# Kernel tuning notes

Hardware: AMD Instinct MI355X
Metric: run time of the kernel (lower is better)

Reference implementation:

```python
import jax, jax.numpy as jnp
import numpy as np

N, E_RAW, F_IN, H, C = 50000, 800000, 500, 5, 32
HID = H * C  # 160
NEG_GAT = 0.2   # GATConv leaky_relu slope for attention logits
NEG = 0.01      # F.leaky_relu default slope
LN_EPS = 1e-5


def glorot(key, shape):
    fan_in, fan_out = shape[0], shape[-1]
    lim = jnp.sqrt(6.0 / (fan_in + fan_out))
    return jax.random.uniform(key, shape, jnp.float32, -lim, lim)


def setup_inputs() -> dict:
    key = jax.random.key(0)
    ks = jax.random.split(key, 12)
    x = jax.random.normal(ks[0], (N, F_IN), jnp.float32)
    edge_index = jax.random.randint(ks[1], (2, E_RAW), 0, N, jnp.int64)
    return {
        "x": x,
        "edge_index": edge_index,
        "W1": glorot(ks[2], (F_IN, HID)),
        "att1_s": glorot(ks[3], (H, C)),
        "att1_d": glorot(ks[4], (H, C)),
        "b1": jnp.zeros((HID,), jnp.float32),
        "g1": jnp.ones((HID,), jnp.float32),
        "be1": jnp.zeros((HID,), jnp.float32),
        "W2": glorot(ks[5], (HID, HID)),
        "att2_s": glorot(ks[6], (H, C)),
        "att2_d": glorot(ks[7], (H, C)),
        "b2": jnp.zeros((HID,), jnp.float32),
        "Wm": glorot(ks[8], (HID, HID)),
        "bm": jnp.zeros((HID,), jnp.float32),
    }


def add_self_loops(edge_index):
    loops = jnp.arange(N, dtype=edge_index.dtype)
    return jnp.concatenate([edge_index, jnp.stack([loops, loops])], axis=1)


def gat_conv(x, src, dst, W, att_s, att_d, bias):
    # x: [N, Fin] -> per-head transform [N, H, C]
    xl = (x @ W).reshape(N, H, C)
    a_s = jnp.einsum('nhc,hc->nh', xl, att_s)  # [N, H]
    a_d = jnp.einsum('nhc,hc->nh', xl, att_d)
    logits = jax.nn.leaky_relu(a_s[src] + a_d[dst], NEG_GAT)  # [E, H]
    # segment softmax over incoming edges of each dst node
    lmax = jax.ops.segment_max(logits, dst, num_segments=N)
    alpha = jnp.exp(logits - lmax[dst])
    denom = jax.ops.segment_sum(alpha, dst, num_segments=N)
    alpha = alpha / (denom[dst] + 1e-16)
    msg = xl[src] * alpha[:, :, None]  # [E, H, C]
    out = jax.ops.segment_sum(msg, dst, num_segments=N)
    return out.reshape(N, HID) + bias, alpha


def layer_norm(x, g, b):
    mu = jnp.mean(x, axis=-1, keepdims=True)
    var = jnp.mean((x - mu) ** 2, axis=-1, keepdims=True)
    return (x - mu) * jax.lax.rsqrt(var + LN_EPS) * g + b


def reference(x, edge_index, W1, att1_s, att1_d, b1, g1, be1,
              W2, att2_s, att2_d, b2, Wm, bm):
    ei = add_self_loops(edge_index)
    src, dst = ei[0], ei[1]
    h, alpha1 = gat_conv(x, src, dst, W1, att1_s, att1_d, b1)
    h = jax.nn.leaky_relu(h, NEG)
    h = layer_norm(h, g1, be1)  # dropout is identity in eval mode
    h, alpha2 = gat_conv(h, src, dst, W2, att2_s, att2_d, b2)
    h = jax.nn.leaky_relu(h, NEG)
    out = jax.nn.leaky_relu(h @ Wm + bm, NEG)
    return out, alpha1, alpha2
```

## Files before the change

### kernel.cpp

```cpp
#include <hip/hip_runtime.h>

#define N_NODES 50000
#define E_RAW_N 800000
#define E_TOT   850000
#define F_IN_K  500
#define HID     160
#define XSTR    184

using short8 = __attribute__((ext_vector_type(8))) short;
using f32x4  = __attribute__((ext_vector_type(4))) float;

__device__ __forceinline__ float b2f(unsigned short u) {
  union { unsigned int i; float f; } v; v.i = ((unsigned int)u) << 16; return v.f;
}
__device__ __forceinline__ unsigned short f2b(float f) {
  union { float f; unsigned int i; } v; v.f = f;
  unsigned int i = v.i;
  unsigned int lsb = (i >> 16) & 1u;
  i += 0x7fffu + lsb;
  return (unsigned short)(i >> 16);
}

__device__ __forceinline__ float wsum(float x) {
  #pragma unroll
  for (int o = 32; o; o >>= 1) x += __shfl_xor(x, o, 64);
  return x;
}
__device__ __forceinline__ float wmax(float x) {
  #pragma unroll
  for (int o = 32; o; o >>= 1) x = fmaxf(x, __shfl_xor(x, o, 64));
  return x;
}
__device__ __forceinline__ float lrelu2(float x) { return x > 0.f ? x : 0.2f * x; }

__global__ void detect_kernel(const int* __restrict__ ei, int* __restrict__ flag) {
  if (threadIdx.x == 0 && blockIdx.x == 0) {
    int allz = 1;
    for (int i = 1; i < 128; i += 2) if (ei[i] != 0) { allz = 0; break; }
    *flag = allz;
  }
}
__device__ __forceinline__ int edge_src(const int* ei, int wide, int e) {
  return wide ? ei[2 * e] : ei[e];
}
__device__ __forceinline__ int edge_dst(const int* ei, int wide, int e) {
  return wide ? ei[2 * (E_RAW_N + e)] : ei[E_RAW_N + e];
}

__global__ __launch_bounds__(256) void convert_all(
    const float* __restrict__ W1, const float* __restrict__ W2, const float* __restrict__ Wm,
    unsigned short* __restrict__ Bt1, unsigned short* __restrict__ Bt2,
    unsigned short* __restrict__ Btm)
{
  const int i = blockIdx.x * 256 + threadIdx.x;
  if (i < HID * 512) {
    const int c = i / 512, k = i % 512;
    Bt1[i] = f2b((k < F_IN_K) ? W1[(long)k * HID + c] : 0.f);
  }
  if (i < HID * 192) {
    const int c = i / 192, k = i % 192;
    Bt2[i] = f2b((k < HID) ? W2[(long)k * HID + c] : 0.f);
    Btm[i] = f2b((k < HID) ? Wm[(long)k * HID + c] : 0.f);
  }
}

template<typename AT, int K, int KPAD, int BK, int MODE>
__global__ __launch_bounds__(128) void gemm_lds(
    const AT* __restrict__ A, const unsigned short* __restrict__ Bt,
    float* __restrict__ C, unsigned short* __restrict__ Ch,
    const float* __restrict__ bias,
    const float* __restrict__ att_s, const float* __restrict__ att_d,
    float* __restrict__ a_d)
{
  constexpr bool AB16 = (sizeof(AT) == 2);
  constexpr int LSTR = BK + 8;
  constexpr int CHUNKS = KPAD / BK;
  constexpr int KSC = BK / 32;
  constexpr int ROWU = BK / 8;
  constexpr int UNITS = HID * ROWU;
  static_assert(UNITS % 128 == 0, "units must tile threads");
  constexpr int UPT = UNITS / 128;
  __shared__ __align__(16) unsigned short Bs[HID][LSTR];

  const int t = threadIdx.x;
  const int l = t & 63;
  const int w = t >> 6;
  const int m = l & 15;
  const int kgrp = (l >> 4) * 8;
  const int rbase = blockIdx.x * 32 + w * 16;
  const int arow = (rbase + m < N_NODES) ? rbase + m : N_NODES - 1;
  const AT* Arow = A + (long)arow * K;

  f32x4 acc[10];
  #pragma unroll
  for (int i = 0; i < 10; ++i) acc[i] = (f32x4){0.f, 0.f, 0.f, 0.f};

  short8 rb[UPT];
  float  arF[KSC][8], arF2[KSC][8];
  short8 arS[KSC], arS2[KSC];

  auto loadB = [&](int cc, short8* dst) {
    #pragma unroll
    for (int i = 0; i < UPT; ++i) {
      const int u = i * 128 + t;
      const int c = u / ROWU;
      const int k8 = u % ROWU;
      dst[i] = *(const short8*)(Bt + (long)c * KPAD + cc * BK + k8 * 8);
    }
  };
  auto loadA = [&](int cc, float aF[KSC][8], short8* aS) {
    #pragma unroll
    for (int ks = 0; ks < KSC; ++ks) {
      const int kb = cc * BK + ks * 32 + kgrp;
      if constexpr (AB16) {
        short8 v = (short8){0,0,0,0,0,0,0,0};
        if (kb + 8 <= K) v = *(const short8*)(Arow + kb);
        else if (kb < K) {
          #pragma unroll
          for (int j = 0; j < 8; ++j) v[j] = (kb + j < K) ? (short)Arow[kb + j] : (short)0;
        }
        aS[ks] = v;
      } else {
        if (kb + 8 <= K) {
          const float4 a0 = *(const float4*)(Arow + kb);
          const float4 a1 = *(const float4*)(Arow + kb + 4);
          aF[ks][0]=a0.x; aF[ks][1]=a0.y; aF[ks][2]=a0.z; aF[ks][3]=a0.w;
          aF[ks][4]=a1.x; aF[ks][5]=a1.y; aF[ks][6]=a1.z; aF[ks][7]=a1.w;
        } else {
          #pragma unroll
          for (int j = 0; j < 8; ++j) aF[ks][j] = (kb + j < K) ? (float)Arow[kb + j] : 0.f;
        }
      }
    }
  };

  loadB(0, rb);
  loadA(0, arF, arS);

  for (int cc = 0; cc < CHUNKS; ++cc) {
    __syncthreads();
    #pragma unroll
    for (int i = 0; i < UPT; ++i) {
      const int u = i * 128 + t;
      const int c = u / ROWU;
      const int k8 = u % ROWU;
      *(short8*)&Bs[c][k8 * 8] = rb[i];
    }
    __syncthreads();
    if (cc + 1 < CHUNKS) {
      loadB(cc + 1, rb);
      loadA(cc + 1, arF2, arS2);
      __builtin_amdgcn_sched_barrier(0);
    }
    __builtin_amdgcn_s_setprio(1);
    #pragma unroll
    for (int ks = 0; ks < KSC; ++ks) {
      short8 ah;
      if constexpr (AB16) {
        ah = arS[ks];
      } else {
        #pragma unroll
        for (int j = 0; j < 8; ++j) ah[j] = (short)f2b(arF[ks][j]);
      }
      #pragma unroll
      for (int ct = 0; ct < 10; ++ct) {
        const short8 bh = *(const short8*)&Bs[ct * 16 + m][ks * 32 + kgrp];
        acc[ct] = __builtin_amdgcn_mfma_f32_16x16x32_bf16(ah, bh, acc[ct], 0, 0, 0);
      }
    }
    __builtin_amdgcn_s_setprio(0);
    if (cc + 1 < CHUNKS) {
      #pragma unroll
      for (int ks = 0; ks < KSC; ++ks) {
        if constexpr (AB16) arS[ks] = arS2[ks];
        else {
          #pragma unroll
          for (int j = 0; j < 8; ++j) arF[ks][j] = arF2[ks][j];
        }
      }
    }
  }

  const int crow0 = rbase + (l >> 4) * 4;

  if (MODE == 2) {
    #pragma unroll
    for (int r = 0; r < 4; ++r) {
      float ps[5], pd[5];
      #pragma unroll
      for (int h = 0; h < 5; ++h) {
        float s = acc[2*h][r]     * att_s[(2*h) * 16 + m]
                + acc[2*h + 1][r] * att_s[(2*h + 1) * 16 + m];
        float d = acc[2*h][r]     * att_d[(2*h) * 16 + m]
                + acc[2*h + 1][r] * att_d[(2*h + 1) * 16 + m];
        #pragma unroll
        for (int o = 1; o < 16; o <<= 1) {
          s += __shfl_xor(s, o, 64);
          d += __shfl_xor(d, o, 64);
        }
        ps[h] = s; pd[h] = d;
      }
      const int crow = crow0 + r;
      if (crow < N_NODES && m < 5) {
        const float vs = m == 0 ? ps[0] : m == 1 ? ps[1] : m == 2 ? ps[2] : m == 3 ? ps[3] : ps[4];
        const float vd = m == 0 ? pd[0] : m == 1 ? pd[1] : m == 2 ? pd[2] : m == 3 ? pd[3] : pd[4];
        ((float*)(Ch + (long)crow * XSTR + 160))[m] = vs;
        a_d[crow * 5 + m] = vd;
      }
    }
  }

  #pragma unroll
  for (int r = 0; r < 4; ++r) {
    const int crow = crow0 + r;
    if (crow < N_NODES) {
      #pragma unroll
      for (int ct = 0; ct < 10; ++ct) {
        const int col = ct * 16 + m;
        float v = acc[ct][r];
        if (MODE == 1) { v += bias[col]; v = v > 0.f ? v : 0.01f * v; }
        if (MODE == 2) Ch[(long)crow * XSTR + col] = f2b(v);
        else           C[(long)crow * HID + col] = v;
      }
    }
  }
}

__global__ __launch_bounds__(256) void count_kernel(const int* __restrict__ ei,
    const int* __restrict__ flag, int* __restrict__ deg) {
  const int e = blockIdx.x * 256 + threadIdx.x;
  if (e >= E_TOT) return;
  const int wide = *flag;
  const int d = (e < E_RAW_N) ? edge_dst(ei, wide, e) : (e - E_RAW_N);
  atomicAdd(&deg[d], 1);
}

#define SCAN_CHUNK 49
__global__ __launch_bounds__(1024) void scan_kernel(const int* __restrict__ deg, int* __restrict__ off) {
  __shared__ int wtot[16];
  const int t = threadIdx.x;
  const int lane = t & 63, wid = t >> 6;
  const int base = t * SCAN_CHUNK;
  int local[SCAN_CHUNK];
  int sum = 0;
  #pragma unroll
  for (int i = 0; i < SCAN_CHUNK; ++i) {
    const int idx = base + i;
    const int v = (idx < N_NODES) ? deg[idx] : 0;
    local[i] = sum;
    sum += v;
  }
  int inc = sum;
  #pragma unroll
  for (int o = 1; o < 64; o <<= 1) {
    const int y = __shfl_up(inc, o, 64);
    if (lane >= o) inc += y;
  }
  if (lane == 63) wtot[wid] = inc;
  __syncthreads();
  if (wid == 0 && lane < 16) {
    const int v = wtot[lane];
    int inc2 = v;
    #pragma unroll
    for (int o = 1; o < 16; o <<= 1) {
      const int y = __shfl_up(inc2, o, 64);
      if (lane >= o) inc2 += y;
    }
    wtot[lane] = inc2 - v;
  }
  __syncthreads();
  const int pre = wtot[wid] + (inc - sum);
  #pragma unroll
  for (int i = 0; i < SCAN_CHUNK; ++i) {
    const int idx = base + i;
    if (idx < N_NODES) off[idx] = pre + local[i];
  }
  if (t == 1023) off[N_NODES] = E_TOT;
}

__global__ __launch_bounds__(256) void fill_kernel(const int* __restrict__ ei,
    const int* __restrict__ flag, const int* __restrict__ off,
    int* __restrict__ fillc, int* __restrict__ csr_src, int* __restrict__ csr_eid) {
  const int e = blockIdx.x * 256 + threadIdx.x;
  if (e >= E_TOT) return;
  const int wide = *flag;
  int s, d;
  if (e < E_RAW_N) { s = edge_src(ei, wide, e); d = edge_dst(ei, wide, e); }
  else { s = e - E_RAW_N; d = s; }
  const int p = off[d] + atomicAdd(&fillc[d], 1);
  csr_src[p] = s;
  csr_eid[p] = e;
}

template<int DO_LN>
__global__ __launch_bounds__(256) void node_kernel(
    const int* __restrict__ off_, const int* __restrict__ csr_src, const int* __restrict__ csr_eid,
    const unsigned short* __restrict__ xlh,
    const float* __restrict__ a_d,
    float* __restrict__ alpha_out,
    const float* __restrict__ bias,
    const float* __restrict__ gamma_, const float* __restrict__ beta_,
    unsigned short* __restrict__ hout)
{
  __shared__ int   srcS[4][64];
  __shared__ float alS[4][64][6];

  const int w = threadIdx.x >> 6;
  const int l = threadIdx.x & 63;
  const int n = blockIdx.x * 4 + w;
  if (n >= N_NODES) return;
  const int off = off_[n];
  const int deg = off_[n + 1] - off;

  const float ad0 = a_d[n*5+0], ad1 = a_d[n*5+1], ad2 = a_d[n*5+2], ad3 = a_d[n*5+3], ad4 = a_d[n*5+4];
  const int hA = l >> 4;
  float accx = 0.f, accy = 0.f, accz = 0.f;

  if (deg <= 64) {
    int src = 0, eid = 0;
    float e0 = 0.f, e1 = 0.f, e2 = 0.f, e3 = 0.f, e4 = 0.f;
    if (l < deg) {
      src = csr_src[off + l];
      eid = csr_eid[off + l];
      const float* ap = (const float*)(xlh + (unsigned)src * XSTR + 160);
      e0 = __expf(lrelu2(ap[0] + ad0));
      e1 = __expf(lrelu2(ap[1] + ad1));
      e2 = __expf(lrelu2(ap[2] + ad2));
      e3 = __expf(lrelu2(ap[3] + ad3));
      e4 = __expf(lrelu2(ap[4] + ad4));
    }
    const float i0 = 1.f / (wsum(e0) + 1e-16f), i1 = 1.f / (wsum(e1) + 1e-16f),
                i2 = 1.f / (wsum(e2) + 1e-16f), i3 = 1.f / (wsum(e3) + 1e-16f),
                i4 = 1.f / (wsum(e4) + 1e-16f);
    const float a0 = e0 * i0, a1 = e1 * i1, a2 = e2 * i2, a3 = e3 * i3, a4 = e4 * i4;
    if (l < deg) {
      float* aw = alpha_out + (long)eid * 5;
      aw[0] = a0; aw[1] = a1; aw[2] = a2; aw[3] = a3; aw[4] = a4;
    }
    srcS[w][l] = src;
    alS[w][l][0] = a0; alS[w][l][1] = a1; alS[w][l][2] = a2;
    alS[w][l][3] = a3; alS[w][l][4] = a4;

    const int degR = (deg + 7) & ~7;
    const unsigned cx = 2 * l, cz = 128 + l;
    for (int s0 = 0; s0 < degR; s0 += 8) {
      int sr[8]; float aA[8], aB[8];
      #pragma unroll
      for (int j = 0; j < 8; ++j) {
        sr[j] = srcS[w][s0 + j];
        aA[j] = alS[w][s0 + j][hA];
        aB[j] = alS[w][s0 + j][4];
      }
      ushort2 u2[8]; unsigned short z[8];
      #pragma unroll
      for (int j = 0; j < 8; ++j) {
        const unsigned xb = (unsigned)sr[j] * XSTR;
        u2[j] = *(const ushort2*)(xlh + xb + cx);
        if (l < 32) z[j] = xlh[xb + cz];
      }
      #pragma unroll
      for (int j = 0; j < 8; ++j) {
        accx += b2f(u2[j].x) * aA[j];
        accy += b2f(u2[j].y) * aA[j];
        if (l < 32) accz += b2f(z[j]) * aB[j];
      }
    }
  } else {
    float m0 = -1e30f, m1 = -1e30f, m2 = -1e30f, m3 = -1e30f, m4 = -1e30f;
    for (int s = l; s < deg; s += 64) {
      const float* ap = (const float*)(xlh + (unsigned)csr_src[off + s] * XSTR + 160);
      m0 = fmaxf(m0, lrelu2(ap[0] + ad0));
      m1 = fmaxf(m1, lrelu2(ap[1] + ad1));
      m2 = fmaxf(m2, lrelu2(ap[2] + ad2));
      m3 = fmaxf(m3, lrelu2(ap[3] + ad3));
      m4 = fmaxf(m4, lrelu2(ap[4] + ad4));
    }
    m0 = wmax(m0); m1 = wmax(m1); m2 = wmax(m2); m3 = wmax(m3); m4 = wmax(m4);
    float s0 = 0.f, s1 = 0.f, s2 = 0.f, s3 = 0.f, s4 = 0.f;
    for (int s = l; s < deg; s += 64) {
      const float* ap = (const float*)(xlh + (unsigned)csr_src[off + s] * XSTR + 160);
      s0 += __expf(lrelu2(ap[0] + ad0) - m0);
      s1 += __expf(lrelu2(ap[1] + ad1) - m1);
      s2 += __expf(lrelu2(ap[2] + ad2) - m2);
      s3 += __expf(lrelu2(ap[3] + ad3) - m3);
      s4 += __expf(lrelu2(ap[4] + ad4) - m4);
    }
    const float i0 = 1.f / (wsum(s0) + 1e-16f), i1 = 1.f / (wsum(s1) + 1e-16f),
                i2 = 1.f / (wsum(s2) + 1e-16f), i3 = 1.f / (wsum(s3) + 1e-16f),
                i4 = 1.f / (wsum(s4) + 1e-16f);
    const float adA = hA == 0 ? ad0 : hA == 1 ? ad1 : hA == 2 ? ad2 : ad3;
    const float mA  = hA == 0 ? m0  : hA == 1 ? m1  : hA == 2 ? m2  : m3;
    const float iA  = hA == 0 ? i0  : hA == 1 ? i1  : hA == 2 ? i2  : i3;
    float adw = 0.f, mw = 0.f, iw = 0.f;
    if (l < 5) {
      adw = l == 0 ? ad0 : l == 1 ? ad1 : l == 2 ? ad2 : l == 3 ? ad3 : ad4;
      mw  = l == 0 ? m0  : l == 1 ? m1  : l == 2 ? m2  : l == 3 ? m3  : m4;
      iw  = l == 0 ? i0  : l == 1 ? i1  : l == 2 ? i2  : l == 3 ? i3  : i4;
    }
    for (int s = 0; s < deg; ++s) {
      const int p = off + s;
      const int srcs = csr_src[p];
      const unsigned xb = (unsigned)srcs * XSTR;
      const float* ap = (const float*)(xlh + xb + 160);
      const float aA = __expf(lrelu2(ap[hA] + adA) - mA) * iA;
      const ushort2 u2 = *(const ushort2*)(xlh + xb + 2 * l);
      accx += b2f(u2.x) * aA;
      accy += b2f(u2.y) * aA;
      if (l < 32) {
        const float aC = __expf(lrelu2(ap[4] + ad4) - m4) * i4;
        accz += b2f(xlh[xb + 128 + l]) * aC;
      }
      if (l < 5) {
        alpha_out[(long)csr_eid[p] * 5 + l] = __expf(lrelu2(ap[l] + adw) - mw) * iw;
      }
    }
  }

  const int c0 = 2 * l, c2 = 128 + l;
  float v0 = accx + bias[c0];     v0 = v0 > 0.f ? v0 : 0.01f * v0;
  float v1 = accy + bias[c0 + 1]; v1 = v1 > 0.f ? v1 : 0.01f * v1;
  float v2 = 0.f;
  if (l < 32) { v2 = accz + bias[c2]; v2 = v2 > 0.f ? v2 : 0.01f * v2; }

  const long hb = (long)n * HID;
  if (DO_LN) {
    const float tot = wsum(v0 + v1 + v2);
    const float mean = tot * (1.f / 160.f);
    const float d0 = v0 - mean, d1 = v1 - mean;
    float sq = d0 * d0 + d1 * d1;
    float d2 = 0.f;
    if (l < 32) { d2 = v2 - mean; sq += d2 * d2; }
    const float var = wsum(sq) * (1.f / 160.f);
    const float rstd = rsqrtf(var + 1e-5f);
    hout[hb + c0]     = f2b(d0 * rstd * gamma_[c0]     + beta_[c0]);
    hout[hb + c0 + 1] = f2b(d1 * rstd * gamma_[c0 + 1] + beta_[c0 + 1]);
    if (l < 32) hout[hb + c2] = f2b(d2 * rstd * gamma_[c2] + beta_[c2]);
  } else {
    hout[hb + c0]     = f2b(v0);
    hout[hb + c0 + 1] = f2b(v1);
    if (l < 32) hout[hb + c2] = f2b(v2);
  }
}

extern "C" void kernel_launch(void* const* d_in, const int* in_sizes, int n_in,
                              void* d_out, int out_size, void* d_ws, size_t ws_size,
                              hipStream_t stream)
{
  const float* x     = (const float*)d_in[0];
  const int*   ei    = (const int*)d_in[1];
  const float* W1    = (const float*)d_in[2];
  const float* att1s = (const float*)d_in[3];
  const float* att1d = (const float*)d_in[4];
  const float* b1    = (const float*)d_in[5];
  const float* g1    = (const float*)d_in[6];
  const float* be1   = (const float*)d_in[7];
  const float* W2    = (const float*)d_in[8];
  const float* att2s = (const float*)d_in[9];
  const float* att2d = (const float*)d_in[10];
  const float* b2    = (const float*)d_in[11];
  const float* Wm    = (const float*)d_in[12];
  const float* bm    = (const float*)d_in[13];

  float* out    = (float*)d_out;
  float* alpha1 = out + (long)N_NODES * HID;
  float* alpha2 = alpha1 + (long)E_TOT * 5;

  char* p = (char*)d_ws;
  auto alloc = [&](size_t bytes) { void* r = (void*)p; p += (bytes + 255) & ~(size_t)255; return r; };
  unsigned short* hb16 = (unsigned short*)alloc((size_t)N_NODES * HID * 2);
  unsigned short* xlh  = (unsigned short*)alloc((size_t)N_NODES * XSTR * 2);
  float* ad_  = (float*)alloc((size_t)N_NODES * 5 * 4);
  int* deg    = (int*)alloc((size_t)N_NODES * 4);
  int* fillc  = (int*)alloc((size_t)N_NODES * 4);
  int* off    = (int*)alloc((size_t)(N_NODES + 1) * 4);
  int* csrS   = (int*)alloc((size_t)E_TOT * 4);
  int* csrE   = (int*)alloc((size_t)E_TOT * 4);
  int* flag   = (int*)alloc(256);
  unsigned short* Bt1 = (unsigned short*)alloc((size_t)HID * 512 * 2);
  unsigned short* Bt2 = (unsigned short*)alloc((size_t)HID * 192 * 2);
  unsigned short* Btm = (unsigned short*)alloc((size_t)HID * 192 * 2);

  hipMemsetAsync(deg, 0, (size_t)N_NODES * 4, stream);
  hipMemsetAsync(fillc, 0, (size_t)N_NODES * 4, stream);

  detect_kernel<<<1, 64, 0, stream>>>(ei, flag);
  const int EB = (E_TOT + 255) / 256;
  count_kernel<<<EB, 256, 0, stream>>>(ei, flag, deg);
  scan_kernel<<<1, 1024, 0, stream>>>(deg, off);
  fill_kernel<<<EB, 256, 0, stream>>>(ei, flag, off, fillc, csrS, csrE);

  convert_all<<<(HID * 512 + 255) / 256, 256, 0, stream>>>(W1, W2, Wm, Bt1, Bt2, Btm);

  const int GB = (N_NODES + 31) / 32;

  gemm_lds<float, F_IN_K, 512, 64, 2><<<GB, 128, 0, stream>>>(x, Bt1, nullptr, xlh, nullptr, att1s, att1d, ad_);
  node_kernel<1><<<N_NODES / 4, 256, 0, stream>>>(off, csrS, csrE, xlh, ad_, alpha1, b1, g1, be1, hb16);

  gemm_lds<unsigned short, HID, 192, 64, 2><<<GB, 128, 0, stream>>>(hb16, Bt2, nullptr, xlh, nullptr, att2s, att2d, ad_);
  node_kernel<0><<<N_NODES / 4, 256, 0, stream>>>(off, csrS, csrE, xlh, ad_, alpha2, b2, nullptr, nullptr, hb16);

  gemm_lds<unsigned short, HID, 192, 64, 1><<<GB, 128, 0, stream>>>(hb16, Btm, out, nullptr, bm, nullptr, nullptr, nullptr);
}
```

Measured before the change: 398.8 us.

## Split GEMM output columns across two wave groups with 256-thread blocks

The LDS-tiled GEMM now launches 256 threads per block. Four waves are arranged as two row groups by two column groups, and each wave computes 5 of the 10 column tiles instead of all 10. This halves the per-wave accumulator count and MFMA chain and doubles the waves per block, aiming for more latency hiding and less register pressure. In return, each A row is loaded twice, and the attention-logit dot products are now partial sums. Those partials are combined through shared memory behind an extra barrier.

```diff
diff --git a/kernel.cpp b/kernel.cpp
--- a/kernel.cpp
+++ b/kernel.cpp
@@ -65,7 +65,7 @@
 }
 
 template<typename AT, int K, int KPAD, int BK, int MODE>
-__global__ __launch_bounds__(128) void gemm_lds(
+__global__ __launch_bounds__(256) void gemm_lds(
     const AT* __restrict__ A, const unsigned short* __restrict__ Bt,
     float* __restrict__ C, unsigned short* __restrict__ Ch,
     const float* __restrict__ bias,
@@ -78,22 +78,25 @@
   constexpr int KSC = BK / 32;
   constexpr int ROWU = BK / 8;
   constexpr int UNITS = HID * ROWU;
-  static_assert(UNITS % 128 == 0, "units must tile threads");
-  constexpr int UPT = UNITS / 128;
+  static_assert(UNITS % 256 == 0, "units must tile threads");
+  constexpr int UPT = UNITS / 256;
   __shared__ __align__(16) unsigned short Bs[HID][LSTR];
+  __shared__ float attP[32][6][2];
 
   const int t = threadIdx.x;
   const int l = t & 63;
   const int w = t >> 6;
+  const int rg = w & 1;
+  const int cg = w >> 1;
   const int m = l & 15;
   const int kgrp = (l >> 4) * 8;
-  const int rbase = blockIdx.x * 32 + w * 16;
+  const int rbase = blockIdx.x * 32 + rg * 16;
   const int arow = (rbase + m < N_NODES) ? rbase + m : N_NODES - 1;
   const AT* Arow = A + (long)arow * K;
 
-  f32x4 acc[10];
-  #pragma unroll
-  for (int i = 0; i < 10; ++i) acc[i] = (f32x4){0.f, 0.f, 0.f, 0.f};
+  f32x4 acc[5];
+  #pragma unroll
+  for (int i = 0; i < 5; ++i) acc[i] = (f32x4){0.f, 0.f, 0.f, 0.f};
 
   short8 rb[UPT];
   float  arF[KSC][8], arF2[KSC][8];
@@ -102,7 +105,7 @@
   auto loadB = [&](int cc, short8* dst) {
     #pragma unroll
     for (int i = 0; i < UPT; ++i) {
-      const int u = i * 128 + t;
+      const int u = i * 256 + t;
       const int c = u / ROWU;
       const int k8 = u % ROWU;
       dst[i] = *(const short8*)(Bt + (long)c * KPAD + cc * BK + k8 * 8);
@@ -141,7 +144,7 @@
     __syncthreads();
     #pragma unroll
     for (int i = 0; i < UPT; ++i) {
-      const int u = i * 128 + t;
+      const int u = i * 256 + t;
       const int c = u / ROWU;
       const int k8 = u % ROWU;
       *(short8*)&Bs[c][k8 * 8] = rb[i];
@@ -163,8 +166,8 @@
         for (int j = 0; j < 8; ++j) ah[j] = (short)f2b(arF[ks][j]);
       }
       #pragma unroll
-      for (int ct = 0; ct < 10; ++ct) {
-        const short8 bh = *(const short8*)&Bs[ct * 16 + m][ks * 32 + kgrp];
+      for (int ct = 0; ct < 5; ++ct) {
+        const short8 bh = *(const short8*)&Bs[(cg * 5 + ct) * 16 + m][ks * 32 + kgrp];
         acc[ct] = __builtin_amdgcn_mfma_f32_16x16x32_bf16(ah, bh, acc[ct], 0, 0, 0);
       }
     }
@@ -184,28 +187,43 @@
   const int crow0 = rbase + (l >> 4) * 4;
 
   if (MODE == 2) {
+    float vsr[4], vdr[4];
     #pragma unroll
     for (int r = 0; r < 4; ++r) {
-      float ps[5], pd[5];
+      float ps[5] = {0.f,0.f,0.f,0.f,0.f}, pd[5] = {0.f,0.f,0.f,0.f,0.f};
+      #pragma unroll
+      for (int ct = 0; ct < 5; ++ct) {
+        const int gct = cg * 5 + ct;
+        const int h = gct >> 1;
+        ps[h] += acc[ct][r] * att_s[gct * 16 + m];
+        pd[h] += acc[ct][r] * att_d[gct * 16 + m];
+      }
       #pragma unroll
       for (int h = 0; h < 5; ++h) {
-        float s = acc[2*h][r]     * att_s[(2*h) * 16 + m]
-                + acc[2*h + 1][r] * att_s[(2*h + 1) * 16 + m];
-        float d = acc[2*h][r]     * att_d[(2*h) * 16 + m]
-                + acc[2*h + 1][r] * att_d[(2*h + 1) * 16 + m];
         #pragma unroll
         for (int o = 1; o < 16; o <<= 1) {
-          s += __shfl_xor(s, o, 64);
-          d += __shfl_xor(d, o, 64);
+          ps[h] += __shfl_xor(ps[h], o, 64);
+          pd[h] += __shfl_xor(pd[h], o, 64);
         }
-        ps[h] = s; pd[h] = d;
-      }
-      const int crow = crow0 + r;
-      if (crow < N_NODES && m < 5) {
-        const float vs = m == 0 ? ps[0] : m == 1 ? ps[1] : m == 2 ? ps[2] : m == 3 ? ps[3] : ps[4];
-        const float vd = m == 0 ? pd[0] : m == 1 ? pd[1] : m == 2 ? pd[2] : m == 3 ? pd[3] : pd[4];
-        ((float*)(Ch + (long)crow * XSTR + 160))[m] = vs;
-        a_d[crow * 5 + m] = vd;
+      }
+      vsr[r] = m == 0 ? ps[0] : m == 1 ? ps[1] : m == 2 ? ps[2] : m == 3 ? ps[3] : ps[4];
+      vdr[r] = m == 0 ? pd[0] : m == 1 ? pd[1] : m == 2 ? pd[2] : m == 3 ? pd[3] : pd[4];
+      const int row_local = rg * 16 + (l >> 4) * 4 + r;
+      if (cg == 1 && m < 5) {
+        attP[row_local][m][0] = vsr[r];
+        attP[row_local][m][1] = vdr[r];
+      }
+    }
+    __syncthreads();
+    if (cg == 0 && m < 5) {
+      #pragma unroll
+      for (int r = 0; r < 4; ++r) {
+        const int crow = crow0 + r;
+        const int row_local = rg * 16 + (l >> 4) * 4 + r;
+        if (crow < N_NODES) {
+          ((float*)(Ch + (long)crow * XSTR + 160))[m] = vsr[r] + attP[row_local][m][0];
+          a_d[crow * 5 + m] = vdr[r] + attP[row_local][m][1];
+        }
       }
     }
   }
@@ -215,8 +233,8 @@
     const int crow = crow0 + r;
     if (crow < N_NODES) {
       #pragma unroll
-      for (int ct = 0; ct < 10; ++ct) {
-        const int col = ct * 16 + m;
+      for (int ct = 0; ct < 5; ++ct) {
+        const int col = (cg * 5 + ct) * 16 + m;
         float v = acc[ct][r];
         if (MODE == 1) { v += bias[col]; v = v > 0.f ? v : 0.01f * v; }
         if (MODE == 2) Ch[(long)crow * XSTR + col] = f2b(v);
@@ -493,11 +511,11 @@
 
   const int GB = (N_NODES + 31) / 32;
 
-  gemm_lds<float, F_IN_K, 512, 64, 2><<<GB, 128, 0, stream>>>(x, Bt1, nullptr, xlh, nullptr, att1s, att1d, ad_);
+  gemm_lds<float, F_IN_K, 512, 64, 2><<<GB, 256, 0, stream>>>(x, Bt1, nullptr, xlh, nullptr, att1s, att1d, ad_);
   node_kernel<1><<<N_NODES / 4, 256, 0, stream>>>(off, csrS, csrE, xlh, ad_, alpha1, b1, g1, be1, hb16);
 
-  gemm_lds<unsigned short, HID, 192, 64, 2><<<GB, 128, 0, stream>>>(hb16, Bt2, nullptr, xlh, nullptr, att2s, att2d, ad_);
+  gemm_lds<unsigned short, HID, 192, 64, 2><<<GB, 256, 0, stream>>>(hb16, Bt2, nullptr, xlh, nullptr, att2s, att2d, ad_);
   node_kernel<0><<<N_NODES / 4, 256, 0, stream>>>(off, csrS, csrE, xlh, ad_, alpha2, b2, nullptr, nullptr, hb16);
 
-  gemm_lds<unsigned short, HID, 192, 64, 1><<<GB, 128, 0, stream>>>(hb16, Btm, out, nullptr, bm, nullptr, nullptr, nullptr);
-}
+  gemm_lds<unsigned short, HID, 192, 64, 1><<<GB, 256, 0, stream>>>(hb16, Btm, out, nullptr, bm, nullptr, nullptr, nullptr);
+}
```

Result: slower. 410.7 us (+3.0%).
